# Optimization experiments

Hardware: AMD Instinct MI355X
Metric: run time of the kernel (lower is better)

## Reference

```python
import jax, jax.numpy as jnp
import numpy as np

EPS = 1e-5  # torch LayerNorm default eps
ALIBI_SLOPE = 1.0

def layer_norm(x, g, b):
    mu = x.mean(-1, keepdims=True)
    var = ((x - mu) ** 2).mean(-1, keepdims=True)
    return (x - mu) * jax.lax.rsqrt(var + EPS) * g + b

def setup_inputs() -> dict:
    key = jax.random.key(0)
    B, T, D, DK, F = 4, 4096, 1024, 128, 2048  # F = ffn_mult * d_model
    ks = jax.random.split(key, 6)
    def s(k, shp, fan):
        return jax.random.normal(k, shp, jnp.float32) / np.sqrt(fan).astype(np.float32)
    return {
        'x': jax.random.normal(ks[0], (B, T, D), jnp.float32),
        'ln1_g': jnp.ones((D,), jnp.float32), 'ln1_b': jnp.zeros((D,), jnp.float32),
        'Wq': s(ks[1], (DK, D), D),  # torch Linear weight layout (out, in)
        'Wk': s(ks[2], (DK, D), D),
        'Wv': s(ks[3], (D, D), D),
        'ln2_g': jnp.ones((D,), jnp.float32), 'ln2_b': jnp.zeros((D,), jnp.float32),
        'W1': s(ks[4], (F, D), D), 'b1': jnp.zeros((F,), jnp.float32),
        'W2': s(ks[5], (D, F), F), 'b2': jnp.zeros((D,), jnp.float32),
    }

def reference(x, ln1_g, ln1_b, Wq, Wk, Wv, ln2_g, ln2_b, W1, b1, W2, b2):
    B, T, D = x.shape
    dk = Wq.shape[0]
    h = layer_norm(x, ln1_g, ln1_b)
    q = jnp.einsum('btd,kd->btk', h, Wq)
    k = jnp.einsum('btd,kd->btk', h, Wk)
    att = jnp.einsum('btk,bsk->bts', q, k) * (dk ** -0.5)  # [B,T,T]
    pos = jnp.arange(T)
    dist = jnp.clip(pos[:, None] - pos[None, :], 0).astype(att.dtype)
    att = att - ALIBI_SLOPE * dist  # alibi bias
    causal = pos[:, None] >= pos[None, :]
    att = jnp.where(causal, att, -jnp.inf)
    att = jax.nn.softmax(att, axis=-1)
    ctx = jnp.einsum('bts,bsd->btd', att, h)  # note: attends over h, not a v-projection
    x = x + jnp.einsum('btd,ed->bte', ctx, Wv)
    h2 = layer_norm(x, ln2_g, ln2_b)
    ff = jnp.maximum(jnp.einsum('btd,fd->btf', h2, W1) + b1, 0.0)
    x = x + jnp.einsum('btf,df->btd', ff, W2) + b2
    return x
```

## Files before the change

kernel.cpp:

```cpp
#include <hip/hip_runtime.h>
#include <stdint.h>

typedef __attribute__((ext_vector_type(4))) float f32x4;
typedef __attribute__((ext_vector_type(8))) unsigned short u16x8;
typedef __attribute__((ext_vector_type(4))) unsigned short u16x4;
typedef unsigned short bf16_t;

#define DEV __device__ __forceinline__

DEV void mfma16(f32x4& d, u16x8 a, u16x8 b) {
    asm("v_mfma_f32_16x16x32_bf16 %0, %1, %2, %0" : "+v"(d) : "v"(a), "v"(b));
}

DEV bf16_t f2bf(float f) {
    uint32_t u = __builtin_bit_cast(uint32_t, f);
    return (bf16_t)((u + 0x7fffu + ((u >> 16) & 1u)) >> 16);
}

DEV void async_g2l16(const void* g, void* l) {
    __builtin_amdgcn_global_load_lds(
        (const __attribute__((address_space(1))) uint32_t*)(uintptr_t)g,
        (__attribute__((address_space(3))) uint32_t*)(uint32_t)(uintptr_t)l,
        16, 0, 0);
}

DEV void blockbar() {
    asm volatile("" ::: "memory");
    __builtin_amdgcn_s_barrier();
    asm volatile("" ::: "memory");
}

#define VMCNT(n) asm volatile("s_waitcnt vmcnt(" #n ")" ::: "memory")

template <int EPI>
__global__ __launch_bounds__(512, 2) void gemm256_nt(
    const bf16_t* __restrict__ A, const bf16_t* __restrict__ B,
    void* __restrict__ Cp, const float* __restrict__ bias,
    const float* __restrict__ res, int M, int N, int K)
{
    __shared__ bf16_t sA[2 * 16384];
    __shared__ bf16_t sB[2 * 16384];
    const int tid = threadIdx.x;
    const int wave = tid >> 6, lane = tid & 63;
    const int lcol = lane & 15, krow = lane >> 4;
    const int wm = wave >> 2, wn = wave & 3;

    int id  = blockIdx.y * gridDim.x + blockIdx.x;
    int nwg = gridDim.x * gridDim.y;
    int swz = ((nwg & 7) == 0) ? ((id & 7) * (nwg >> 3) + (id >> 3)) : id;
    const int bn = swz % gridDim.y;
    const int bm = swz / gridDim.y;
    const int row_a = bm * 256, col_c = bn * 256;

    const int trow = tid >> 3;
    const int tr = (((tid & 7) ^ ((tid >> 3) & 7)) * 8);
    const bf16_t* aSt = A + (size_t)(row_a + trow) * K + tr;
    const bf16_t* bSt = B + (size_t)(col_c + trow) * K + tr;
    const size_t rstep = (size_t)64 * K;
    bf16_t* ldsAw = sA + wave * 512;
    bf16_t* ldsBw = sB + wave * 512;

    const int rowA = wm * 128 + lcol;
    const int rowB = wn * 64  + lcol;
    const int cA0 = ((krow ^ (rowA & 7))) * 8;
    const int cB0 = ((krow ^ (rowB & 7))) * 8;
    const int aBase = rowA * 64 + cA0;
    const int bBase = rowB * 64 + cB0;

    f32x4 acc[8][4] = {};
    const int nt = K >> 6;

#pragma unroll
    for (int i = 0; i < 4; i++) {
        async_g2l16(aSt + (size_t)i * rstep, ldsAw + i * 4096);
        async_g2l16(bSt + (size_t)i * rstep, ldsBw + i * 4096);
    }
    VMCNT(0);
    blockbar();

    for (int t = 0; t < nt; ++t) {
        const int rbase = (t & 1) ? 16384 : 0;
        const int wbase = 16384 - rbase;
        const bool pf = (t + 1) < nt;
        const size_t ko = (size_t)(t + 1) * 64;

        if (pf) {
#pragma unroll
            for (int i = 0; i < 4; i++) {
                async_g2l16(aSt + ko + (size_t)i * rstep, ldsAw + wbase + i * 4096);
                async_g2l16(bSt + ko + (size_t)i * rstep, ldsBw + wbase + i * 4096);
            }
        }

        u16x8 fa[8], fb[4];
#pragma unroll
        for (int mi = 0; mi < 8; mi++) fa[mi] = *(const u16x8*)&sA[rbase + aBase + mi * 1024];
#pragma unroll
        for (int ni = 0; ni < 4; ni++) fb[ni] = *(const u16x8*)&sB[rbase + bBase + ni * 1024];
#pragma unroll
        for (int mi = 0; mi < 8; mi++)
#pragma unroll
            for (int ni = 0; ni < 4; ni++)
                mfma16(acc[mi][ni], fa[mi], fb[ni]);
#pragma unroll
        for (int mi = 0; mi < 8; mi++) fa[mi] = *(const u16x8*)&sA[rbase + ((aBase + mi * 1024) ^ 32)];
#pragma unroll
        for (int ni = 0; ni < 4; ni++) fb[ni] = *(const u16x8*)&sB[rbase + ((bBase + ni * 1024) ^ 32)];
#pragma unroll
        for (int mi = 0; mi < 8; mi++)
#pragma unroll
            for (int ni = 0; ni < 4; ni++)
                mfma16(acc[mi][ni], fa[mi], fb[ni]);

        VMCNT(0);
        blockbar();
    }

#pragma unroll
    for (int mi = 0; mi < 8; mi++)
#pragma unroll
        for (int ni = 0; ni < 4; ni++)
#pragma unroll
            for (int j = 0; j < 4; j++) {
                const int gr = row_a + wm * 128 + mi * 16 + krow * 4 + j;
                const int gc = col_c + wn * 64 + ni * 16 + lcol;
                float v = acc[mi][ni][j];
                if (EPI == 0) {
                    ((bf16_t*)Cp)[(size_t)gr * N + gc] = f2bf(v);
                } else if (EPI == 1) {
                    v += bias[gc];
                    v = fmaxf(v, 0.f);
                    ((bf16_t*)Cp)[(size_t)gr * N + gc] = f2bf(v);
                } else if (EPI == 2) {
                    ((float*)Cp)[(size_t)gr * N + gc] = v + res[(size_t)gr * N + gc];
                } else {
                    ((float*)Cp)[(size_t)gr * N + gc] = v + bias[gc] + res[(size_t)gr * N + gc];
                }
            }
}

template <int EPI>
__global__ __launch_bounds__(256) void gemm_nt(
    const bf16_t* __restrict__ A, const bf16_t* __restrict__ B,
    void* __restrict__ Cp, const float* __restrict__ bias,
    const float* __restrict__ res, int M, int N, int K)
{
    alignas(16) __shared__ bf16_t sA[128 * 32];
    alignas(16) __shared__ bf16_t sB[128 * 32];
    const int tid = threadIdx.x;
    const int wave = tid >> 6, lane = tid & 63;
    const int lcol = lane & 15, krow = lane >> 4;

    int id  = blockIdx.y * gridDim.x + blockIdx.x;
    int nwg = gridDim.x * gridDim.y;
    int swz = ((nwg & 7) == 0) ? ((id & 7) * (nwg >> 3) + (id >> 3)) : id;
    const int bn = swz % gridDim.y;
    const int bm = swz / gridDim.y;

    const int row_a = bm * 128, col_c = bn * 128;
    const int wm = (wave >> 1) * 64, wn = (wave & 1) * 64;

    const int   srow  = wave * 16 + (lane >> 2);
    const int   scol  = (lane & 3) * 8;
    const bf16_t* aSrc = A + (size_t)(row_a + srow) * K + scol;
    const bf16_t* bSrc = B + (size_t)(col_c + srow) * K + scol;
    char* sAl = (char*)sA + wave * 1024;
    char* sBl = (char*)sB + wave * 1024;
    const size_t rstep = (size_t)64 * K;

    f32x4 acc[4][4] = {};

    for (int k0 = 0; k0 < K; k0 += 32) {
        async_g2l16(aSrc + k0,         sAl);
        async_g2l16(aSrc + k0 + rstep, sAl + 4096);
        async_g2l16(bSrc + k0,         sBl);
        async_g2l16(bSrc + k0 + rstep, sBl + 4096);
        __syncthreads();
        u16x8 af[4], bfr[4];
#pragma unroll
        for (int i = 0; i < 4; i++) {
            af[i]  = *(const u16x8*)&sA[(wm + i * 16 + lcol) * 32 + krow * 8];
            bfr[i] = *(const u16x8*)&sB[(wn + i * 16 + lcol) * 32 + krow * 8];
        }
#pragma unroll
        for (int mi = 0; mi < 4; mi++)
#pragma unroll
            for (int ni = 0; ni < 4; ni++)
                mfma16(acc[mi][ni], af[mi], bfr[ni]);
        __syncthreads();
    }

#pragma unroll
    for (int mi = 0; mi < 4; mi++)
#pragma unroll
        for (int ni = 0; ni < 4; ni++)
#pragma unroll
            for (int j = 0; j < 4; j++) {
                const int gr = row_a + wm + mi * 16 + krow * 4 + j;
                const int gc = col_c + wn + ni * 16 + lcol;
                float v = acc[mi][ni][j];
                if (EPI == 0) {
                    ((bf16_t*)Cp)[(size_t)gr * N + gc] = f2bf(v);
                } else if (EPI == 1) {
                    v += bias[gc];
                    v = fmaxf(v, 0.f);
                    ((bf16_t*)Cp)[(size_t)gr * N + gc] = f2bf(v);
                } else if (EPI == 2) {
                    ((float*)Cp)[(size_t)gr * N + gc] = v + res[(size_t)gr * N + gc];
                } else {
                    ((float*)Cp)[(size_t)gr * N + gc] = v + bias[gc] + res[(size_t)gr * N + gc];
                }
            }
}

__global__ __launch_bounds__(256) void ln_kernel(
    const float* __restrict__ X, const float* __restrict__ G,
    const float* __restrict__ Bt, bf16_t* __restrict__ O)
{
    const int row = blockIdx.x, tid = threadIdx.x;
    const int wave = tid >> 6, lane = tid & 63;
    const size_t base = (size_t)row * 1024 + tid * 4;
    f32x4 xv = *(const f32x4*)&X[base];
    float s  = xv[0] + xv[1] + xv[2] + xv[3];
    float s2 = xv[0]*xv[0] + xv[1]*xv[1] + xv[2]*xv[2] + xv[3]*xv[3];
#pragma unroll
    for (int o = 1; o < 64; o <<= 1) { s += __shfl_xor(s, o); s2 += __shfl_xor(s2, o); }
    __shared__ float red[8];
    if (lane == 0) { red[wave] = s; red[wave + 4] = s2; }
    __syncthreads();
    s  = red[0] + red[1] + red[2] + red[3];
    s2 = red[4] + red[5] + red[6] + red[7];
    const float mu = s * (1.f / 1024.f);
    const float rs = rsqrtf(s2 * (1.f / 1024.f) - mu * mu + 1e-5f);
    f32x4 gv = *(const f32x4*)&G[tid * 4];
    f32x4 bv = *(const f32x4*)&Bt[tid * 4];
    u16x4 ov;
#pragma unroll
    for (int i = 0; i < 4; i++) ov[i] = f2bf((xv[i] - mu) * rs * gv[i] + bv[i]);
    *(u16x4*)&O[base] = ov;
}

__global__ __launch_bounds__(256) void cvt_f32_bf16(
    const float* __restrict__ src, bf16_t* __restrict__ dst, int n)
{
    int i = (blockIdx.x * 256 + threadIdx.x) * 4;
    if (i >= n) return;
    f32x4 v = *(const f32x4*)&src[i];
    u16x4 o;
#pragma unroll
    for (int t = 0; t < 4; t++) o[t] = f2bf(v[t]);
    *(u16x4*)&dst[i] = o;
}

__global__ __launch_bounds__(256) void attn_p(
    const bf16_t* __restrict__ QK, bf16_t* __restrict__ P, int T)
{
    const int tid = threadIdx.x, w = tid >> 6, lane = tid & 63;
    const int lcol = lane & 15, krow = lane >> 4;
    const int qt = blockIdx.x;
    const int ntb = T >> 6;
    const int b = qt / ntb;
    const int r0 = (qt - b * ntb) << 6;
    const size_t g0 = (size_t)b * T + r0;
    const int jbase = r0 - 192;
    const float scale = 0.08838834764831845f;

    __shared__ float lred[2][4][64];

    u16x8 qf[4][4];
#pragma unroll
    for (int mf = 0; mf < 4; mf++)
#pragma unroll
        for (int ks = 0; ks < 4; ks++)
            qf[mf][ks] = *(const u16x8*)&QK[(g0 + mf * 16 + lcol) * 256 + ks * 32 + krow * 8];

    f32x4 acc[4][4] = {};
    const size_t kbase = (size_t)b * T * 256 + 128;
#pragma unroll
    for (int ks = 0; ks < 4; ks++) {
        u16x8 kf[4];
#pragma unroll
        for (int nf = 0; nf < 4; nf++) {
            int jc = jbase + w * 64 + nf * 16 + lcol;
            int jr = jc < 0 ? 0 : jc;
            kf[nf] = *(const u16x8*)&QK[kbase + (size_t)jr * 256 + ks * 32 + krow * 8];
        }
#pragma unroll
        for (int mf = 0; mf < 4; mf++)
#pragma unroll
            for (int nf = 0; nf < 4; nf++)
                mfma16(acc[mf][nf], qf[mf][ks], kf[nf]);
    }

#pragma unroll
    for (int mf = 0; mf < 4; mf++)
#pragma unroll
        for (int j = 0; j < 4; j++) {
            const int i_ = r0 + mf * 16 + krow * 4 + j;
            float m = -1e30f;
#pragma unroll
            for (int nf = 0; nf < 4; nf++) {
                const int jc = jbase + w * 64 + nf * 16 + lcol;
                float sv = (jc >= 0 && jc <= i_) ? acc[mf][nf][j] * scale - (float)(i_ - jc) : -1e30f;
                acc[mf][nf][j] = sv;
                m = fmaxf(m, sv);
            }
#pragma unroll
            for (int o = 1; o < 16; o <<= 1) m = fmaxf(m, __shfl_xor(m, o));
            if (lcol == 0) lred[0][w][mf * 16 + krow * 4 + j] = m;
        }
    __syncthreads();

#pragma unroll
    for (int mf = 0; mf < 4; mf++)
#pragma unroll
        for (int j = 0; j < 4; j++) {
            const int rr = mf * 16 + krow * 4 + j;
            const float m = fmaxf(fmaxf(lred[0][0][rr], lred[0][1][rr]),
                                  fmaxf(lred[0][2][rr], lred[0][3][rr]));
            float sm = 0.f;
#pragma unroll
            for (int nf = 0; nf < 4; nf++) {
                float p = __expf(acc[mf][nf][j] - m);
                acc[mf][nf][j] = p;
                sm += p;
            }
#pragma unroll
            for (int o = 1; o < 16; o <<= 1) sm += __shfl_xor(sm, o);
            if (lcol == 0) lred[1][w][rr] = sm;
        }
    __syncthreads();

    float inv_l[4][4];
#pragma unroll
    for (int mf = 0; mf < 4; mf++)
#pragma unroll
        for (int j = 0; j < 4; j++) {
            const int rr = mf * 16 + krow * 4 + j;
            inv_l[mf][j] = 1.f / (lred[1][0][rr] + lred[1][1][rr] + lred[1][2][rr] + lred[1][3][rr]);
        }
#pragma unroll
    for (int mf = 0; mf < 4; mf++)
#pragma unroll
        for (int nf = 0; nf < 4; nf++)
#pragma unroll
            for (int j = 0; j < 4; j++) {
                const int rr = mf * 16 + krow * 4 + j;
                P[((size_t)qt * 64 + rr) * 256 + w * 64 + nf * 16 + lcol] =
                    f2bf(acc[mf][nf][j] * inv_l[mf][j]);
            }
}

__global__ __launch_bounds__(256) void pv_gemm(
    const bf16_t* __restrict__ P, const bf16_t* __restrict__ H,
    bf16_t* __restrict__ CTX, int T)
{
    alignas(16) __shared__ bf16_t sHt[128 * 40];
    const int tid = threadIdx.x, w = tid >> 6, lane = tid & 63;
    const int lcol = lane & 15, krow = lane >> 4;
    const int qt = blockIdx.x, d0 = blockIdx.y * 128;
    const int ntb = T >> 6, b = qt / ntb;
    const int r0 = (qt - b * ntb) << 6;
    const int jbase = r0 - 192;
    const int wm = (w >> 1) * 32, wn = (w & 1) * 64;
    const int kk = tid >> 3, seg = tid & 7;

    f32x4 acc[2][4] = {};
    for (int k0 = 0; k0 < 256; k0 += 32) {
        int j = jbase + k0 + kk;
        if (j < 0) j = 0;
        const bf16_t* hp = H + ((size_t)b * T + j) * 1024 + d0 + seg * 16;
        u16x8 v0 = *(const u16x8*)hp;
        u16x8 v1 = *(const u16x8*)(hp + 8);
        __syncthreads();
#pragma unroll
        for (int i = 0; i < 8; i++) {
            sHt[(seg * 16 + i) * 40 + kk]     = v0[i];
            sHt[(seg * 16 + 8 + i) * 40 + kk] = v1[i];
        }
        __syncthreads();
        u16x8 af[2], bfr[4];
#pragma unroll
        for (int mi = 0; mi < 2; mi++)
            af[mi] = *(const u16x8*)&P[((size_t)qt * 64 + wm + mi * 16 + lcol) * 256 + k0 + krow * 8];
#pragma unroll
        for (int ni = 0; ni < 4; ni++)
            bfr[ni] = *(const u16x8*)&sHt[(wn + ni * 16 + lcol) * 40 + krow * 8];
#pragma unroll
        for (int mi = 0; mi < 2; mi++)
#pragma unroll
            for (int ni = 0; ni < 4; ni++)
                mfma16(acc[mi][ni], af[mi], bfr[ni]);
    }
#pragma unroll
    for (int mi = 0; mi < 2; mi++)
#pragma unroll
        for (int ni = 0; ni < 4; ni++)
#pragma unroll
            for (int j = 0; j < 4; j++)
                CTX[((size_t)b * T + r0 + wm + mi * 16 + krow * 4 + j) * 1024 +
                    d0 + wn + ni * 16 + lcol] = f2bf(acc[mi][ni][j]);
}

extern "C" void kernel_launch(void* const* d_in, const int* in_sizes, int n_in,
                              void* d_out, int out_size, void* d_ws, size_t ws_size,
                              hipStream_t stream)
{
    const float* x   = (const float*)d_in[0];
    const float* g1  = (const float*)d_in[1];
    const float* be1 = (const float*)d_in[2];
    const float* Wq  = (const float*)d_in[3];
    const float* Wk  = (const float*)d_in[4];
    const float* Wv  = (const float*)d_in[5];
    const float* g2  = (const float*)d_in[6];
    const float* be2 = (const float*)d_in[7];
    const float* W1  = (const float*)d_in[8];
    const float* b1  = (const float*)d_in[9];
    const float* W2  = (const float*)d_in[10];
    const float* b2  = (const float*)d_in[11];

    const int B = 4, T = 4096, D = 1024, DK = 128, F = 2048;
    const int BT = B * T;

    char* ws = (char*)d_ws;
    size_t off = 0;
    auto alloc = [&](size_t bytes) {
        void* p = ws + off;
        off += (bytes + 255) & ~(size_t)255;
        return p;
    };
    bf16_t* wqk_b = (bf16_t*)alloc((size_t)2 * DK * D * 2);
    bf16_t* wv_b  = (bf16_t*)alloc((size_t)D * D * 2);
    bf16_t* w1_b  = (bf16_t*)alloc((size_t)F * D * 2);
    bf16_t* w2_b  = (bf16_t*)alloc((size_t)D * F * 2);
    bf16_t* h     = (bf16_t*)alloc((size_t)BT * D * 2);
    bf16_t* qk    = (bf16_t*)alloc((size_t)BT * 256 * 2);
    bf16_t* P     = (bf16_t*)alloc((size_t)BT * 256 * 2);
    bf16_t* ctx   = (bf16_t*)alloc((size_t)BT * D * 2);
    bf16_t* ff    = (bf16_t*)alloc((size_t)BT * F * 2);
    if (ws_size < off) return;
    float* x2 = (float*)d_out;

    cvt_f32_bf16<<<DK * D / 1024, 256, 0, stream>>>(Wq, wqk_b, DK * D);
    cvt_f32_bf16<<<DK * D / 1024, 256, 0, stream>>>(Wk, wqk_b + (size_t)DK * D, DK * D);
    cvt_f32_bf16<<<D * D / 1024, 256, 0, stream>>>(Wv, wv_b, D * D);
    cvt_f32_bf16<<<F * D / 1024, 256, 0, stream>>>(W1, w1_b, F * D);
    cvt_f32_bf16<<<D * F / 1024, 256, 0, stream>>>(W2, w2_b, D * F);

    ln_kernel<<<BT, 256, 0, stream>>>(x, g1, be1, h);

    gemm_nt<0><<<dim3(BT / 128, 2), 256, 0, stream>>>(h, wqk_b, qk, nullptr, nullptr, BT, 256, D);

    attn_p<<<BT / 64, 256, 0, stream>>>(qk, P, T);
    pv_gemm<<<dim3(BT / 64, D / 128), 256, 0, stream>>>(P, h, ctx, T);

    gemm256_nt<2><<<dim3(BT / 256, D / 256), 512, 0, stream>>>(ctx, wv_b, x2, nullptr, x, BT, D, D);

    ln_kernel<<<BT, 256, 0, stream>>>(x2, g2, be2, h);

    gemm256_nt<1><<<dim3(BT / 256, F / 256), 512, 0, stream>>>(h, w1_b, ff, b1, nullptr, BT, F, D);

    gemm256_nt<3><<<dim3(BT / 256, D / 256), 512, 0, stream>>>(ff, w2_b, x2, b2, x2, BT, D, F);
}
```

Measured before the change: 336.0 us.

## Reassociate value projection before PV and fuse weight conversion with LayerNorm

Precomputes G = h·Wvᵀ as a full GEMM, then has the banded PV kernel multiply P by G and add the residual x directly into the fp32 output. This drops the separate ctx buffer and the residual-fused Wv GEMM after attention. The five weight-conversion kernels and the first LayerNorm are merged into one launch to cut launch overhead. Rounding G to bf16 before the attention-weighted sum changes numerics slightly, and the merged kernel relies on the converted weights sitting contiguously in the workspace.

```diff
diff --git a/kernel.cpp b/kernel.cpp
--- a/kernel.cpp
+++ b/kernel.cpp
@@ -240,16 +240,51 @@
     *(u16x4*)&O[base] = ov;
 }
 
-__global__ __launch_bounds__(256) void cvt_f32_bf16(
-    const float* __restrict__ src, bf16_t* __restrict__ dst, int n)
-{
-    int i = (blockIdx.x * 256 + threadIdx.x) * 4;
-    if (i >= n) return;
-    f32x4 v = *(const f32x4*)&src[i];
-    u16x4 o;
-#pragma unroll
-    for (int t = 0; t < 4; t++) o[t] = f2bf(v[t]);
-    *(u16x4*)&dst[i] = o;
+__global__ __launch_bounds__(256) void cvt_ln(
+    const float* __restrict__ s0, const float* __restrict__ s1,
+    const float* __restrict__ s2, const float* __restrict__ s3,
+    const float* __restrict__ s4, bf16_t* __restrict__ wdst,
+    int n0, int n1, int n2, int n3, int n4, int ncvtblk,
+    const float* __restrict__ X, const float* __restrict__ G,
+    const float* __restrict__ Bt, bf16_t* __restrict__ O)
+{
+    const int tid = threadIdx.x;
+    if ((int)blockIdx.x < ncvtblk) {
+        int i = (blockIdx.x * 256 + tid) * 4;
+        const float* sp; int base;
+        if (i < n0)                     { sp = s0; base = 0; }
+        else if (i < n0+n1)             { sp = s1; base = n0; }
+        else if (i < n0+n1+n2)          { sp = s2; base = n0+n1; }
+        else if (i < n0+n1+n2+n3)       { sp = s3; base = n0+n1+n2; }
+        else                            { sp = s4; base = n0+n1+n2+n3; }
+        f32x4 v = *(const f32x4*)&sp[i - base];
+        u16x4 o;
+#pragma unroll
+        for (int t = 0; t < 4; t++) o[t] = f2bf(v[t]);
+        *(u16x4*)&wdst[i] = o;
+        return;
+    }
+    const int row = blockIdx.x - ncvtblk;
+    const int wave = tid >> 6, lane = tid & 63;
+    const size_t base = (size_t)row * 1024 + tid * 4;
+    f32x4 xv = *(const f32x4*)&X[base];
+    float sum = xv[0] + xv[1] + xv[2] + xv[3];
+    float ssq = xv[0]*xv[0] + xv[1]*xv[1] + xv[2]*xv[2] + xv[3]*xv[3];
+#pragma unroll
+    for (int o = 1; o < 64; o <<= 1) { sum += __shfl_xor(sum, o); ssq += __shfl_xor(ssq, o); }
+    __shared__ float red[8];
+    if (lane == 0) { red[wave] = sum; red[wave + 4] = ssq; }
+    __syncthreads();
+    sum = red[0] + red[1] + red[2] + red[3];
+    ssq = red[4] + red[5] + red[6] + red[7];
+    const float mu = sum * (1.f / 1024.f);
+    const float rs = rsqrtf(ssq * (1.f / 1024.f) - mu * mu + 1e-5f);
+    f32x4 gv = *(const f32x4*)&G[tid * 4];
+    f32x4 bv = *(const f32x4*)&Bt[tid * 4];
+    u16x4 ov;
+#pragma unroll
+    for (int i = 0; i < 4; i++) ov[i] = f2bf((xv[i] - mu) * rs * gv[i] + bv[i]);
+    *(u16x4*)&O[base] = ov;
 }
 
 __global__ __launch_bounds__(256) void attn_p(
@@ -351,9 +386,9 @@
             }
 }
 
-__global__ __launch_bounds__(256) void pv_gemm(
-    const bf16_t* __restrict__ P, const bf16_t* __restrict__ H,
-    bf16_t* __restrict__ CTX, int T)
+__global__ __launch_bounds__(256) void pv2_gemm(
+    const bf16_t* __restrict__ P, const bf16_t* __restrict__ Gm,
+    const float* __restrict__ X, float* __restrict__ X2, int T)
 {
     alignas(16) __shared__ bf16_t sHt[128 * 40];
     const int tid = threadIdx.x, w = tid >> 6, lane = tid & 63;
@@ -369,7 +404,7 @@
     for (int k0 = 0; k0 < 256; k0 += 32) {
         int j = jbase + k0 + kk;
         if (j < 0) j = 0;
-        const bf16_t* hp = H + ((size_t)b * T + j) * 1024 + d0 + seg * 16;
+        const bf16_t* hp = Gm + ((size_t)b * T + j) * 1024 + d0 + seg * 16;
         u16x8 v0 = *(const u16x8*)hp;
         u16x8 v1 = *(const u16x8*)(hp + 8);
         __syncthreads();
@@ -397,9 +432,11 @@
 #pragma unroll
         for (int ni = 0; ni < 4; ni++)
 #pragma unroll
-            for (int j = 0; j < 4; j++)
-                CTX[((size_t)b * T + r0 + wm + mi * 16 + krow * 4 + j) * 1024 +
-                    d0 + wn + ni * 16 + lcol] = f2bf(acc[mi][ni][j]);
+            for (int j = 0; j < 4; j++) {
+                const size_t oi = ((size_t)b * T + r0 + wm + mi * 16 + krow * 4 + j) * 1024 +
+                                  d0 + wn + ni * 16 + lcol;
+                X2[oi] = X[oi] + acc[mi][ni][j];
+            }
 }
 
 extern "C" void kernel_launch(void* const* d_in, const int* in_sizes, int n_in,
@@ -436,25 +473,23 @@
     bf16_t* h     = (bf16_t*)alloc((size_t)BT * D * 2);
     bf16_t* qk    = (bf16_t*)alloc((size_t)BT * 256 * 2);
     bf16_t* P     = (bf16_t*)alloc((size_t)BT * 256 * 2);
-    bf16_t* ctx   = (bf16_t*)alloc((size_t)BT * D * 2);
+    bf16_t* G     = (bf16_t*)alloc((size_t)BT * D * 2);
     bf16_t* ff    = (bf16_t*)alloc((size_t)BT * F * 2);
     if (ws_size < off) return;
     float* x2 = (float*)d_out;
 
-    cvt_f32_bf16<<<DK * D / 1024, 256, 0, stream>>>(Wq, wqk_b, DK * D);
-    cvt_f32_bf16<<<DK * D / 1024, 256, 0, stream>>>(Wk, wqk_b + (size_t)DK * D, DK * D);
-    cvt_f32_bf16<<<D * D / 1024, 256, 0, stream>>>(Wv, wv_b, D * D);
-    cvt_f32_bf16<<<F * D / 1024, 256, 0, stream>>>(W1, w1_b, F * D);
-    cvt_f32_bf16<<<D * F / 1024, 256, 0, stream>>>(W2, w2_b, D * F);
-
-    ln_kernel<<<BT, 256, 0, stream>>>(x, g1, be1, h);
+    const int n0 = DK * D, n2 = D * D, n3 = F * D, n4 = D * F;
+    const int ncvtblk = (n0 + n0 + n2 + n3 + n4) / 1024;
+    cvt_ln<<<ncvtblk + BT, 256, 0, stream>>>(Wq, Wk, Wv, W1, W2, wqk_b,
+                                             n0, n0, n2, n3, n4, ncvtblk,
+                                             x, g1, be1, h);
 
     gemm_nt<0><<<dim3(BT / 128, 2), 256, 0, stream>>>(h, wqk_b, qk, nullptr, nullptr, BT, 256, D);
 
+    gemm256_nt<0><<<dim3(BT / 256, D / 256), 512, 0, stream>>>(h, wv_b, G, nullptr, nullptr, BT, D, D);
+
     attn_p<<<BT / 64, 256, 0, stream>>>(qk, P, T);
-    pv_gemm<<<dim3(BT / 64, D / 128), 256, 0, stream>>>(P, h, ctx, T);
-
-    gemm256_nt<2><<<dim3(BT / 256, D / 256), 512, 0, stream>>>(ctx, wv_b, x2, nullptr, x, BT, D, D);
+    pv2_gemm<<<dim3(BT / 64, D / 128), 256, 0, stream>>>(P, G, x, x2, T);
 
     ln_kernel<<<BT, 256, 0, stream>>>(x2, g2, be2, h);
 
```

Measured after the change: 330.1 us. About the same (-1.8%).
